# Kernel tuning notes

Hardware: AMD Instinct MI355X
Metric: run time of the kernel (lower is better)

The kernel has to match this reference:

```python
import jax, jax.numpy as jnp
import numpy as np

T, D_IN, H, D_OUT = 20, 4, 768, 1
B = 1024


def setup_inputs() -> dict:
    key = jax.random.key(0)
    ks = jax.random.split(key, 8)
    s = 1.0 / np.sqrt(H)
    return {
        "batch_price": jax.random.normal(ks[0], (B, T, D_IN), jnp.float32),
        "batch_event": jax.random.normal(ks[1], (B, T, H), jnp.float32),
        "W_ih": jax.random.uniform(ks[2], (T, 4 * H, D_IN), jnp.float32, -s, s),
        "W_hh": jax.random.uniform(ks[3], (T, 4 * H, H), jnp.float32, -s, s),
        "b_ih": jax.random.uniform(ks[4], (T, 4 * H), jnp.float32, -s, s),
        "b_hh": jax.random.uniform(ks[5], (T, 4 * H), jnp.float32, -s, s),
        "fc_w": jax.random.uniform(ks[6], (D_OUT, H), jnp.float32, -s, s),
        "fc_b": jax.random.uniform(ks[7], (D_OUT,), jnp.float32, -s, s),
    }


def _lstm_cell(x, h_mat, c, wih, whh, bih, bhh):
    # gates: [B, 4H] in PyTorch LSTMCell order (i, f, g, o)
    gates = x @ wih.T + bih + h_mat @ whh.T + bhh
    i, f, g, o = jnp.split(gates, 4, axis=-1)
    c_next = jax.nn.sigmoid(f) * c + jax.nn.sigmoid(i) * jnp.tanh(g)
    h_next = jax.nn.sigmoid(o) * jnp.tanh(c_next)
    return h_next, c_next


def reference(batch_price, batch_event, W_ih, W_hh, b_ih, b_hh, fc_w, fc_b):
    Bb, Tt, _ = batch_price.shape
    Hh = W_hh.shape[-1]
    # step 0: hx = batch_event[:, 0], cell state = zeros
    h, c = _lstm_cell(batch_price[:, 0], batch_event[:, 0],
                      jnp.zeros((Bb, Hh), batch_price.dtype),
                      W_ih[0], W_hh[0], b_ih[0], b_hh[0])

    def step(carry, inp):
        h, c = carry
        x, ev, wih, whh, bih, bhh = inp
        # faithful to source: hx = torch.sum(batch_event_t + h_prev) -> scalar
        hx = jnp.sum(ev + h)
        h_mat = jnp.broadcast_to(hx, (Bb, Hh))
        h2, c2 = _lstm_cell(x, h_mat, c, wih, whh, bih, bhh)
        return (h2, c2), None

    xs = (jnp.swapaxes(batch_price[:, 1:], 0, 1),  # [T-1, B, D_IN]
          jnp.swapaxes(batch_event[:, 1:], 0, 1),  # [T-1, B, H]
          W_ih[1:], W_hh[1:], b_ih[1:], b_hh[1:])
    (h, c), _ = jax.lax.scan(step, (h, c), xs)
    return h @ fc_w.T + fc_b  # [B, 1]
```

## Files before the change

kernel.cpp:

```cpp
#include <hip/hip_runtime.h>
#include <stdint.h>

#define Bsz 1024
#define Tn  20
#define Hn  768
#define G4n 3072

#define WS_SH    0
#define WS_SEV   32
#define WS_PART  64
#define WS_BCAST 576
#define WS_RS    640
#define WS_BS    (640 + Tn*G4n)
#define WS_C     (640 + 2*Tn*G4n)

#define NB_GEMM   768
#define NB_ROWSUM 14592
#define NB_BIAS   240
#define NB_SEV    1216
#define NB_TOTAL  (NB_GEMM + NB_ROWSUM + NB_BIAS + NB_SEV)

typedef float  floatx4 __attribute__((ext_vector_type(4)));
typedef short  bfrag8  __attribute__((ext_vector_type(8)));

__device__ __forceinline__ float wave_reduce(float v){
#pragma unroll
    for (int o = 32; o > 0; o >>= 1) v += __shfl_down(v, o, 64);
    return v;
}
__device__ __forceinline__ float sigf(float x){ return 1.0f/(1.0f+__expf(-x)); }
__device__ __forceinline__ float tanhfast(float x){ return 2.0f/(1.0f+__expf(-2.0f*x)) - 1.0f; }
__device__ __forceinline__ unsigned short f2bf(float f){
    uint32_t u = __float_as_uint(f);
    return (unsigned short)((u + 0x7fffu + ((u>>16)&1u)) >> 16);
}
__device__ __forceinline__ float bf2f(unsigned short h){ return __uint_as_float(((uint32_t)h)<<16); }
__device__ __forceinline__ uint64_t pack_tv(unsigned t, float v){
    return ((uint64_t)t << 32) | (uint64_t)__float_as_uint(v);
}

__global__ void k_init(float* __restrict__ ws){
    if (threadIdx.x < 640) ws[threadIdx.x] = 0.0f;
}

__global__ __launch_bounds__(256) void k_pre(
    const float* __restrict__ price, const float* __restrict__ ev,
    const float* __restrict__ wih,   const float* __restrict__ whh,
    const float* __restrict__ bih,   const float* __restrict__ bhh,
    float* __restrict__ ws)
{
    __shared__ __align__(16) char smraw[4*64*56*2 + 16];
    unsigned short* Ah = (unsigned short*)smraw;
    unsigned short* Al = Ah + 64*56;
    unsigned short* Bh = Al + 64*56;
    unsigned short* Bl = Bh + 64*56;
    float* redk = (float*)(smraw + 4*64*56*2);
    float* red  = (float*)smraw;

    int blk = blockIdx.x, tid = threadIdx.x;

    if (blk < NB_GEMM) {
        float* Sh   = ws + WS_SH;
        float* cbuf = ws + WS_C;
        int bt = blk / 48, kt = blk % 48;
        int b0 = bt*64, k0 = kt*16;
        int w = tid >> 6, lane = tid & 63;
        int q = lane >> 4, col = lane & 15;

        int srow = tid >> 2;
        int kkoff = (tid & 3) * 8;
        int g_s = srow >> 4, rr = srow & 15;
        const float* aRow = ev  + (size_t)(b0 + srow)*(Tn*Hn);
        const float* bRow = whh + (size_t)(g_s*Hn + k0 + rr)*Hn;

        floatx4 acc[4];
#pragma unroll
        for (int g = 0; g < 4; ++g) acc[g] = (floatx4){0.f,0.f,0.f,0.f};

        for (int kk0 = 0; kk0 < Hn; kk0 += 32) {
            {
                const float* p = aRow + kk0 + kkoff;
                float4 v0 = *(const float4*)p;
                float4 v1 = *(const float4*)(p+4);
                float f[8] = {v0.x,v0.y,v0.z,v0.w,v1.x,v1.y,v1.z,v1.w};
                bfrag8 hv, lv;
#pragma unroll
                for (int i = 0; i < 8; ++i) {
                    unsigned short hb = f2bf(f[i]);
                    hv[i] = (short)hb;
                    lv[i] = (short)f2bf(f[i] - bf2f(hb));
                }
                *(bfrag8*)&Ah[srow*56 + kkoff] = hv;
                *(bfrag8*)&Al[srow*56 + kkoff] = lv;
                const float* pb = bRow + kk0 + kkoff;
                float4 u0 = *(const float4*)pb;
                float4 u1 = *(const float4*)(pb+4);
                float fb[8] = {u0.x,u0.y,u0.z,u0.w,u1.x,u1.y,u1.z,u1.w};
#pragma unroll
                for (int i = 0; i < 8; ++i) {
                    unsigned short hb = f2bf(fb[i]);
                    hv[i] = (short)hb;
                    lv[i] = (short)f2bf(fb[i] - bf2f(hb));
                }
                *(bfrag8*)&Bh[srow*56 + kkoff] = hv;
                *(bfrag8*)&Bl[srow*56 + kkoff] = lv;
            }
            __syncthreads();

            bfrag8 ah = *(const bfrag8*)&Ah[(w*16 + col)*56 + q*8];
            bfrag8 al = *(const bfrag8*)&Al[(w*16 + col)*56 + q*8];
#pragma unroll
            for (int g = 0; g < 4; ++g) {
                bfrag8 bh = *(const bfrag8*)&Bh[(g*16 + col)*56 + q*8];
                bfrag8 bl = *(const bfrag8*)&Bl[(g*16 + col)*56 + q*8];
                acc[g] = __builtin_amdgcn_mfma_f32_16x16x32_bf16(ah, bh, acc[g], 0,0,0);
                acc[g] = __builtin_amdgcn_mfma_f32_16x16x32_bf16(ah, bl, acc[g], 0,0,0);
                acc[g] = __builtin_amdgcn_mfma_f32_16x16x32_bf16(al, bh, acc[g], 0,0,0);
            }
            __syncthreads();
        }

        float hsum = 0.f;
#pragma unroll
        for (int r = 0; r < 4; ++r) {
            int b = b0 + w*16 + q*4 + r;
            float4 xv = *(const float4*)(price + (size_t)b*(Tn*4));
            float gates[4];
#pragma unroll
            for (int g = 0; g < 4; ++g) {
                int j = g*Hn + k0 + col;
                float4 wv = *(const float4*)(wih + (size_t)j*4);
                gates[g] = acc[g][r] + xv.x*wv.x + xv.y*wv.y + xv.z*wv.z + xv.w*wv.w
                         + bih[j] + bhh[j];
            }
            float c0 = sigf(gates[0]) * tanhfast(gates[2]);
            float h0 = sigf(gates[3]) * tanhfast(c0);
            cbuf[(size_t)b*Hn + k0 + col] = c0;
            hsum += h0;
        }
        hsum = wave_reduce(hsum);
        if (lane == 0) redk[w] = hsum;
        __syncthreads();
        if (tid == 0) atomicAdd(&Sh[0], redk[0]+redk[1]+redk[2]+redk[3]);
        return;
    }

    blk -= NB_GEMM;
    float* Sev     = ws + WS_SEV;
    float* rowsum  = ws + WS_RS;
    float* biassum = ws + WS_BS;

    if (blk < NB_ROWSUM) {
        int r    = blk*4 + (tid>>6);
        int lane = tid & 63;
        int t    = 1 + r/G4n;
        int j    = r - (t-1)*G4n;
        const float* base = whh + (size_t)t*G4n*Hn + (size_t)j*Hn;
        float s = 0.f;
#pragma unroll
        for (int i = 0; i < 3; ++i) {
            float4 v = *(const float4*)(base + (size_t)(lane + 64*i)*4);
            s += v.x + v.y + v.z + v.w;
        }
        s = wave_reduce(s);
        if (lane == 0) rowsum[t*G4n + j] = s;
    } else if (blk < NB_ROWSUM + NB_BIAS) {
        int idx = (blk - NB_ROWSUM)*256 + tid;
        if (idx < Tn*G4n) biassum[idx] = bih[idx] + bhh[idx];
    } else {
        int sb = blk - NB_ROWSUM - NB_BIAS;
        int t  = 1 + (sb >> 6);
        int b0 = (sb & 63) * 16;
        float s = 0.f;
        for (int bb = 0; bb < 16; ++bb) {
            const float* base = ev + (size_t)(b0+bb)*(Tn*Hn) + (size_t)t*Hn;
            s += base[tid] + base[tid+256] + base[tid+512];
        }
        s = wave_reduce(s);
        if ((tid & 63) == 0) red[tid>>6] = s;
        __syncthreads();
        if (tid == 0) atomicAdd(&Sev[t], red[0]+red[1]+red[2]+red[3]);
    }
}

__global__ __launch_bounds__(768) void k_steps(
    const float* __restrict__ price, const float* __restrict__ wih,
    const float* __restrict__ fcw,   const float* __restrict__ fcb,
    float* __restrict__ ws, float* __restrict__ out)
{
    __shared__ float pr[4][80];
    __shared__ float red[12];
    __shared__ float redP[4];
    __shared__ float redF[4][12];
    __shared__ float shx;

    float* Sh  = ws + WS_SH;
    float* Sev = ws + WS_SEV;
    uint64_t* part  = (uint64_t*)(ws + WS_PART);
    uint64_t* bcast = (uint64_t*)(ws + WS_BCAST);
    const float* rowsum  = ws + WS_RS;
    const float* biassum = ws + WS_BS;
    float* cbuf = ws + WS_C;

    int blk = blockIdx.x, tid = threadIdx.x;
    int lane = tid & 63, wid = tid >> 6;
    int k = tid;

    if (tid < 320) {
        int e = tid / 80, r = tid - e*80;
        pr[e][r] = price[(size_t)(blk + 256*e)*(Tn*4) + r];
    }

    float c[4];
#pragma unroll
    for (int e = 0; e < 4; ++e)
        c[e] = cbuf[(size_t)(blk + 256*e)*Hn + k];

    float fcwk = fcw[k];
    float fcb0 = fcb[0];

    float hsum_prev = 0.f;
    float vout[4] = {0.f,0.f,0.f,0.f};

    for (int t = 1; t < Tn; ++t) {
        const float* wih_t = wih + (size_t)t*G4n*4;
        float rsv[4], base[4][4];
#pragma unroll
        for (int g = 0; g < 4; ++g) {
            int j = g*Hn + k;
            float4 wv = *(const float4*)(wih_t + (size_t)j*4);
            rsv[g]   = rowsum[t*G4n + j];
            float bs = biassum[t*G4n + j];
#pragma unroll
            for (int e = 0; e < 4; ++e) {
                base[e][g] = pr[e][t*4+0]*wv.x + pr[e][t*4+1]*wv.y
                           + pr[e][t*4+2]*wv.z + pr[e][t*4+3]*wv.w + bs;
            }
        }

        if (t >= 2) {
            float v = wave_reduce(hsum_prev);
            if (lane == 0) red[wid] = v;
            __syncthreads();
            if (tid == 0) {
                float tot = 0.f;
#pragma unroll
                for (int i = 0; i < 12; ++i) tot += red[i];
                __hip_atomic_store(&part[blk], pack_tv((unsigned)(t-1), tot),
                                   __ATOMIC_RELAXED, __HIP_MEMORY_SCOPE_AGENT);
            }
        }

        if (blk == 0) {
            if (t >= 2) {
                if (tid < 256) {
                    uint64_t u;
                    do { u = __hip_atomic_load(&part[tid], __ATOMIC_RELAXED, __HIP_MEMORY_SCOPE_AGENT); }
                    while ((unsigned)(u >> 32) != (unsigned)(t-1));
                    float pv = wave_reduce(__uint_as_float((uint32_t)u));
                    if (lane == 0) redP[wid] = pv;
                }
                __syncthreads();
                if (tid == 0) {
                    float Shprev = redP[0]+redP[1]+redP[2]+redP[3];
                    float hx = Sev[t] + Shprev;
                    shx = hx;
                    __hip_atomic_store(bcast, pack_tv((unsigned)t, hx),
                                       __ATOMIC_RELAXED, __HIP_MEMORY_SCOPE_AGENT);
                }
            } else {
                if (tid == 0) {
                    float hx = Sev[1] + Sh[0];
                    shx = hx;
                    __hip_atomic_store(bcast, pack_tv(1u, hx),
                                       __ATOMIC_RELAXED, __HIP_MEMORY_SCOPE_AGENT);
                }
            }
            __syncthreads();
        } else {
            if (tid == 0) {
                uint64_t u;
                do { u = __hip_atomic_load(bcast, __ATOMIC_RELAXED, __HIP_MEMORY_SCOPE_AGENT); }
                while ((unsigned)(u >> 32) != (unsigned)t);
                shx = __uint_as_float((uint32_t)u);
            }
            __syncthreads();
        }
        float hx = shx;

        float hsum = 0.f;
#pragma unroll
        for (int e = 0; e < 4; ++e) {
            float gi = base[e][0] + hx*rsv[0];
            float gf = base[e][1] + hx*rsv[1];
            float gg = base[e][2] + hx*rsv[2];
            float go = base[e][3] + hx*rsv[3];
            float cn = sigf(gf)*c[e] + sigf(gi)*tanhfast(gg);
            c[e] = cn;
            float h = sigf(go)*tanhfast(cn);
            hsum += h;
            if (t == Tn-1) vout[e] = wave_reduce(h * fcwk);
        }
        hsum_prev = hsum;
    }

    if (lane == 0) {
#pragma unroll
        for (int e = 0; e < 4; ++e) redF[e][wid] = vout[e];
    }
    __syncthreads();
    if (tid < 4) {
        float tot = 0.f;
#pragma unroll
        for (int i = 0; i < 12; ++i) tot += redF[tid][i];
        out[blk + 256*tid] = tot + fcb0;
    }
}

extern "C" void kernel_launch(void* const* d_in, const int* in_sizes, int n_in,
                              void* d_out, int out_size, void* d_ws, size_t ws_size,
                              hipStream_t stream)
{
    const float* price = (const float*)d_in[0];
    const float* ev    = (const float*)d_in[1];
    const float* wih   = (const float*)d_in[2];
    const float* whh   = (const float*)d_in[3];
    const float* bih   = (const float*)d_in[4];
    const float* bhh   = (const float*)d_in[5];
    const float* fcw   = (const float*)d_in[6];
    const float* fcb   = (const float*)d_in[7];
    float* out = (float*)d_out;
    float* ws  = (float*)d_ws;

    k_init<<<1, 640, 0, stream>>>(ws);
    k_pre <<<NB_TOTAL, 256, 0, stream>>>(price, ev, wih, whh, bih, bhh, ws);
    k_steps<<<256, 768, 0, stream>>>(price, wih, fcw, fcb, ws, out);
}
```

Measured before the change: 419.3 us.

## Replace leader-broadcast barrier with all-to-all partial reads, split rowsum kernel

The step loop's per-timestep barrier no longer funnels through block 0 and a broadcast slot. Every block now publishes its partial sum into a double-buffered slot array and reads all 256 partials itself, which removes one global round trip per step. The W_hh row-sum work moves into its own kernel where each wave handles four rows, and the bf16 hi/lo split now truncates instead of rounding to nearest. The cost is more global polling traffic per step and one extra kernel launch.

```diff
diff --git a/kernel.cpp b/kernel.cpp
--- a/kernel.cpp
+++ b/kernel.cpp
@@ -9,16 +9,15 @@
 #define WS_SH    0
 #define WS_SEV   32
 #define WS_PART  64
-#define WS_BCAST 576
-#define WS_RS    640
-#define WS_BS    (640 + Tn*G4n)
-#define WS_C     (640 + 2*Tn*G4n)
+#define WS_RS    1088
+#define WS_BS    (1088 + Tn*G4n)
+#define WS_C     (1088 + 2*Tn*G4n)
 
 #define NB_GEMM   768
-#define NB_ROWSUM 14592
 #define NB_BIAS   240
 #define NB_SEV    1216
-#define NB_TOTAL  (NB_GEMM + NB_ROWSUM + NB_BIAS + NB_SEV)
+#define NB_A      (NB_GEMM + NB_BIAS + NB_SEV)
+#define NB_ROWSUM 3648
 
 typedef float  floatx4 __attribute__((ext_vector_type(4)));
 typedef short  bfrag8  __attribute__((ext_vector_type(8)));
@@ -30,9 +29,8 @@
 }
 __device__ __forceinline__ float sigf(float x){ return 1.0f/(1.0f+__expf(-x)); }
 __device__ __forceinline__ float tanhfast(float x){ return 2.0f/(1.0f+__expf(-2.0f*x)) - 1.0f; }
-__device__ __forceinline__ unsigned short f2bf(float f){
-    uint32_t u = __float_as_uint(f);
-    return (unsigned short)((u + 0x7fffu + ((u>>16)&1u)) >> 16);
+__device__ __forceinline__ unsigned short f2bf_t(float f){
+    return (unsigned short)(__float_as_uint(f) >> 16);
 }
 __device__ __forceinline__ float bf2f(unsigned short h){ return __uint_as_float(((uint32_t)h)<<16); }
 __device__ __forceinline__ uint64_t pack_tv(unsigned t, float v){
@@ -40,10 +38,10 @@
 }
 
 __global__ void k_init(float* __restrict__ ws){
-    if (threadIdx.x < 640) ws[threadIdx.x] = 0.0f;
-}
-
-__global__ __launch_bounds__(256) void k_pre(
+    for (int i = threadIdx.x; i < 1088; i += 1024) ws[i] = 0.0f;
+}
+
+__global__ __launch_bounds__(256) void k_gemm_sev(
     const float* __restrict__ price, const float* __restrict__ ev,
     const float* __restrict__ wih,   const float* __restrict__ whh,
     const float* __restrict__ bih,   const float* __restrict__ bhh,
@@ -86,9 +84,9 @@
                 bfrag8 hv, lv;
 #pragma unroll
                 for (int i = 0; i < 8; ++i) {
-                    unsigned short hb = f2bf(f[i]);
+                    unsigned short hb = f2bf_t(f[i]);
                     hv[i] = (short)hb;
-                    lv[i] = (short)f2bf(f[i] - bf2f(hb));
+                    lv[i] = (short)f2bf_t(f[i] - bf2f(hb));
                 }
                 *(bfrag8*)&Ah[srow*56 + kkoff] = hv;
                 *(bfrag8*)&Al[srow*56 + kkoff] = lv;
@@ -98,9 +96,9 @@
                 float fb[8] = {u0.x,u0.y,u0.z,u0.w,u1.x,u1.y,u1.z,u1.w};
 #pragma unroll
                 for (int i = 0; i < 8; ++i) {
-                    unsigned short hb = f2bf(fb[i]);
+                    unsigned short hb = f2bf_t(fb[i]);
                     hv[i] = (short)hb;
-                    lv[i] = (short)f2bf(fb[i] - bf2f(hb));
+                    lv[i] = (short)f2bf_t(fb[i] - bf2f(hb));
                 }
                 *(bfrag8*)&Bh[srow*56 + kkoff] = hv;
                 *(bfrag8*)&Bl[srow*56 + kkoff] = lv;
@@ -141,34 +139,19 @@
         hsum = wave_reduce(hsum);
         if (lane == 0) redk[w] = hsum;
         __syncthreads();
-        if (tid == 0) atomicAdd(&Sh[0], redk[0]+redk[1]+redk[2]+redk[3]);
+        if (tid == 0) atomicAdd(&ws[WS_SH], redk[0]+redk[1]+redk[2]+redk[3]);
         return;
     }
 
     blk -= NB_GEMM;
     float* Sev     = ws + WS_SEV;
-    float* rowsum  = ws + WS_RS;
     float* biassum = ws + WS_BS;
 
-    if (blk < NB_ROWSUM) {
-        int r    = blk*4 + (tid>>6);
-        int lane = tid & 63;
-        int t    = 1 + r/G4n;
-        int j    = r - (t-1)*G4n;
-        const float* base = whh + (size_t)t*G4n*Hn + (size_t)j*Hn;
-        float s = 0.f;
-#pragma unroll
-        for (int i = 0; i < 3; ++i) {
-            float4 v = *(const float4*)(base + (size_t)(lane + 64*i)*4);
-            s += v.x + v.y + v.z + v.w;
-        }
-        s = wave_reduce(s);
-        if (lane == 0) rowsum[t*G4n + j] = s;
-    } else if (blk < NB_ROWSUM + NB_BIAS) {
-        int idx = (blk - NB_ROWSUM)*256 + tid;
+    if (blk < NB_BIAS) {
+        int idx = blk*256 + tid;
         if (idx < Tn*G4n) biassum[idx] = bih[idx] + bhh[idx];
     } else {
-        int sb = blk - NB_ROWSUM - NB_BIAS;
+        int sb = blk - NB_BIAS;
         int t  = 1 + (sb >> 6);
         int b0 = (sb & 63) * 16;
         float s = 0.f;
@@ -180,6 +163,33 @@
         if ((tid & 63) == 0) red[tid>>6] = s;
         __syncthreads();
         if (tid == 0) atomicAdd(&Sev[t], red[0]+red[1]+red[2]+red[3]);
+    }
+}
+
+__global__ __launch_bounds__(256) void k_rowsum(
+    const float* __restrict__ whh, float* __restrict__ ws)
+{
+    float* rowsum = ws + WS_RS;
+    int tid = threadIdx.x, lane = tid & 63, wid = tid >> 6;
+    int r0 = blockIdx.x*16 + wid*4;
+    int t  = 1 + r0/G4n;
+    int j0 = r0 - (t-1)*G4n;
+    const float* base = whh + (size_t)t*G4n*Hn + (size_t)j0*Hn;
+
+    float s[4];
+#pragma unroll
+    for (int rr = 0; rr < 4; ++rr) {
+        const float* p = base + (size_t)rr*Hn + lane*4;
+        float4 a = *(const float4*)p;
+        float4 b = *(const float4*)(p + 256);
+        float4 c = *(const float4*)(p + 512);
+        s[rr] = (a.x+a.y)+(a.z+a.w) + (b.x+b.y)+(b.z+b.w) + (c.x+c.y)+(c.z+c.w);
+    }
+#pragma unroll
+    for (int rr = 0; rr < 4; ++rr) s[rr] = wave_reduce(s[rr]);
+    if (lane == 0) {
+#pragma unroll
+        for (int rr = 0; rr < 4; ++rr) rowsum[t*G4n + j0 + rr] = s[rr];
     }
 }
 
@@ -192,12 +202,10 @@
     __shared__ float red[12];
     __shared__ float redP[4];
     __shared__ float redF[4][12];
-    __shared__ float shx;
 
     float* Sh  = ws + WS_SH;
     float* Sev = ws + WS_SEV;
-    uint64_t* part  = (uint64_t*)(ws + WS_PART);
-    uint64_t* bcast = (uint64_t*)(ws + WS_BCAST);
+    uint64_t* part = (uint64_t*)(ws + WS_PART);
     const float* rowsum  = ws + WS_RS;
     const float* biassum = ws + WS_BS;
     float* cbuf = ws + WS_C;
@@ -218,6 +226,7 @@
 
     float fcwk = fcw[k];
     float fcb0 = fcb[0];
+    __syncthreads();
 
     float hsum_prev = 0.f;
     float vout[4] = {0.f,0.f,0.f,0.f};
@@ -238,7 +247,11 @@
             }
         }
 
-        if (t >= 2) {
+        float hx;
+        if (t == 1) {
+            hx = Sev[1] + Sh[0];
+        } else {
+            int ph = (t-1) & 1;
             float v = wave_reduce(hsum_prev);
             if (lane == 0) red[wid] = v;
             __syncthreads();
@@ -246,47 +259,19 @@
                 float tot = 0.f;
 #pragma unroll
                 for (int i = 0; i < 12; ++i) tot += red[i];
-                __hip_atomic_store(&part[blk], pack_tv((unsigned)(t-1), tot),
+                __hip_atomic_store(&part[ph*256 + blk], pack_tv((unsigned)(t-1), tot),
                                    __ATOMIC_RELAXED, __HIP_MEMORY_SCOPE_AGENT);
             }
-        }
-
-        if (blk == 0) {
-            if (t >= 2) {
-                if (tid < 256) {
-                    uint64_t u;
-                    do { u = __hip_atomic_load(&part[tid], __ATOMIC_RELAXED, __HIP_MEMORY_SCOPE_AGENT); }
-                    while ((unsigned)(u >> 32) != (unsigned)(t-1));
-                    float pv = wave_reduce(__uint_as_float((uint32_t)u));
-                    if (lane == 0) redP[wid] = pv;
-                }
-                __syncthreads();
-                if (tid == 0) {
-                    float Shprev = redP[0]+redP[1]+redP[2]+redP[3];
-                    float hx = Sev[t] + Shprev;
-                    shx = hx;
-                    __hip_atomic_store(bcast, pack_tv((unsigned)t, hx),
-                                       __ATOMIC_RELAXED, __HIP_MEMORY_SCOPE_AGENT);
-                }
-            } else {
-                if (tid == 0) {
-                    float hx = Sev[1] + Sh[0];
-                    shx = hx;
-                    __hip_atomic_store(bcast, pack_tv(1u, hx),
-                                       __ATOMIC_RELAXED, __HIP_MEMORY_SCOPE_AGENT);
-                }
+            if (tid < 256) {
+                uint64_t u;
+                do { u = __hip_atomic_load(&part[ph*256 + tid], __ATOMIC_RELAXED, __HIP_MEMORY_SCOPE_AGENT); }
+                while ((unsigned)(u >> 32) != (unsigned)(t-1));
+                float pv = wave_reduce(__uint_as_float((uint32_t)u));
+                if (lane == 0) redP[wid] = pv;
             }
             __syncthreads();
-        } else {
-            if (tid == 0) {
-                uint64_t u;
-                do { u = __hip_atomic_load(bcast, __ATOMIC_RELAXED, __HIP_MEMORY_SCOPE_AGENT); }
-                while ((unsigned)(u >> 32) != (unsigned)t);
-                shx = __uint_as_float((uint32_t)u);
-            }
-            __syncthreads();
-        }
-        float hx = shx;
+            hx = Sev[t] + ((redP[0]+redP[1]) + (redP[2]+redP[3]));
+        }
 
         float hsum = 0.f;
 #pragma unroll
@@ -332,7 +317,8 @@
     float* out = (float*)d_out;
     float* ws  = (float*)d_ws;
 
-    k_init<<<1, 640, 0, stream>>>(ws);
-    k_pre <<<NB_TOTAL, 256, 0, stream>>>(price, ev, wih, whh, bih, bhh, ws);
-    k_steps<<<256, 768, 0, stream>>>(price, wih, fcw, fcb, ws, out);
-}
+    k_init    <<<1, 1024, 0, stream>>>(ws);
+    k_rowsum  <<<NB_ROWSUM, 256, 0, stream>>>(whh, ws);
+    k_gemm_sev<<<NB_A, 256, 0, stream>>>(price, ev, wih, whh, bih, bhh, ws);
+    k_steps   <<<256, 768, 0, stream>>>(price, wih, fcw, fcb, ws, out);
+}
```

Measured after the change: 443.8 us. 1.06x slower.
